# Optimization experiments

Hardware: AMD Instinct MI355X
Metric: run time of the kernel (lower is better)

## Reference

```python
import jax, jax.numpy as jnp
import numpy as np

SEQ_LEN = 4096
N_FEATURES = 1
EMB = 768
HID = 2 * EMB


def _lstm(x, Wih, Whh, bih, bhh):
    """PyTorch-semantics single-layer LSTM over x: [S, in] -> (hs [S, H], h_N [H]).
    Gate order: i, f, g, o. Zero initial state."""
    H = Whh.shape[1]
    # Precompute the input contribution for all timesteps (one big GEMM).
    xW = x @ Wih.T + (bih + bhh)  # [S, 4H]

    def step(carry, g_in):
        h, c = carry
        gates = g_in + Whh @ h  # [4H]
        i, f, g, o = jnp.split(gates, 4)
        c = jax.nn.sigmoid(f) * c + jax.nn.sigmoid(i) * jnp.tanh(g)
        h = jax.nn.sigmoid(o) * jnp.tanh(c)
        return (h, c), h

    init = (jnp.zeros((H,), x.dtype), jnp.zeros((H,), x.dtype))
    (hN, _), hs = jax.lax.scan(step, init, xW)
    return hs, hN


def setup_inputs() -> dict:
    key = jax.random.key(0)
    ks = iter(jax.random.split(key, 32))

    def u(shape, H):
        b = 1.0 / np.sqrt(H)  # PyTorch LSTM/Linear init: U(-1/sqrt(H), 1/sqrt(H))
        return jax.random.uniform(next(ks), shape, jnp.float32, -b, b)

    def lstm_params(in_dim, H):
        return (u((4 * H, in_dim), H), u((4 * H, H), H), u((4 * H,), H), u((4 * H,), H))

    e1_Wih, e1_Whh, e1_bih, e1_bhh = lstm_params(N_FEATURES, HID)
    e2_Wih, e2_Whh, e2_bih, e2_bhh = lstm_params(HID, EMB)
    d1_Wih, d1_Whh, d1_bih, d1_bhh = lstm_params(EMB, EMB)
    d2_Wih, d2_Whh, d2_bih, d2_bhh = lstm_params(EMB, HID)
    out_W = u((N_FEATURES, HID), HID)
    out_b = u((N_FEATURES,), HID)

    x = jax.random.normal(next(ks), (SEQ_LEN, N_FEATURES), jnp.float32)
    return dict(x=x,
                e1_Wih=e1_Wih, e1_Whh=e1_Whh, e1_bih=e1_bih, e1_bhh=e1_bhh,
                e2_Wih=e2_Wih, e2_Whh=e2_Whh, e2_bih=e2_bih, e2_bhh=e2_bhh,
                d1_Wih=d1_Wih, d1_Whh=d1_Whh, d1_bih=d1_bih, d1_bhh=d1_bhh,
                d2_Wih=d2_Wih, d2_Whh=d2_Whh, d2_bih=d2_bih, d2_bhh=d2_bhh,
                out_W=out_W, out_b=out_b)


def reference(x,
              e1_Wih, e1_Whh, e1_bih, e1_bhh,
              e2_Wih, e2_Whh, e2_bih, e2_bhh,
              d1_Wih, d1_Whh, d1_bih, d1_bhh,
              d2_Wih, d2_Whh, d2_bih, d2_bhh,
              out_W, out_b):
    x = x.reshape(SEQ_LEN, N_FEATURES)
    h1, _ = _lstm(x, e1_Wih, e1_Whh, e1_bih, e1_bhh)          # [S, HID]
    _, z = _lstm(h1, e2_Wih, e2_Whh, e2_bih, e2_bhh)          # [EMB] bottleneck
    zrep = jnp.broadcast_to(z, (SEQ_LEN, EMB))                # repeat across time
    d1, _ = _lstm(zrep, d1_Wih, d1_Whh, d1_bih, d1_bhh)       # [S, EMB]
    d2, _ = _lstm(d1, d2_Wih, d2_Whh, d2_bih, d2_bhh)         # [S, HID]
    return d2 @ out_W.T + out_b                               # [S, N_FEATURES]
```

## Files before the change

kernel.cpp:

```cpp
#include <hip/hip_runtime.h>
#include <math.h>
#include <stdint.h>

#define SEQ   4096
#define NWG   256
#define NTHR  256
#define FINTAG 0x40000000u

#define WS_BIG  0
#define WS_SML  12288
#define WS_FIN  18432
#define WS_OUTP 18944
#define WS_ZERO WS_OUTP

typedef float f32x4 __attribute__((ext_vector_type(4)));
typedef float f32x2 __attribute__((ext_vector_type(2)));

__device__ __forceinline__ float sigf(float x){
  float e = __builtin_amdgcn_exp2f(-1.44269504089f * x);
  return __builtin_amdgcn_rcpf(1.0f + e);
}
__device__ __forceinline__ float tanhf_fast(float x){
  float e = __builtin_amdgcn_exp2f(2.88539008178f * x);
  return 1.0f - 2.0f * __builtin_amdgcn_rcpf(e + 1.0f);
}

__device__ __forceinline__ float wsum64(float v){
#pragma unroll
  for (int m = 32; m > 0; m >>= 1) v += __shfl_xor(v, m);
  return v;
}

__device__ __forceinline__ float g_load(const float* p){
  return __hip_atomic_load(p, __ATOMIC_RELAXED, __HIP_MEMORY_SCOPE_AGENT);
}
__device__ __forceinline__ void g_store(float* p, float v){
  __hip_atomic_store(p, v, __ATOMIC_RELAXED, __HIP_MEMORY_SCOPE_AGENT);
}
__device__ __forceinline__ void cell_store(float* cell, float h, unsigned tag){
  unsigned long long pk = ((unsigned long long)tag << 32) | (unsigned long long)__float_as_uint(h);
  __hip_atomic_store((unsigned long long*)cell, pk, __ATOMIC_RELAXED, __HIP_MEMORY_SCOPE_AGENT);
}

#define DOT4(acc, wv4, hv4) \
  acc += (wv4)[0]*(hv4)[0] + (wv4)[1]*(hv4)[1] + (wv4)[2]*(hv4)[2] + (wv4)[3]*(hv4)[3];

#define RETRY_BIG(bbp, tgv)                                                  \
  for(;;){                                                                   \
    asm volatile(                                                            \
      "global_load_dwordx4 %0, %3, off sc0 sc1\n\t"                          \
      "global_load_dwordx4 %1, %3, off offset:1024 sc0 sc1\n\t"              \
      "global_load_dwordx4 %2, %3, off offset:2048 sc0 sc1\n\t"              \
      "s_waitcnt vmcnt(0)"                                                   \
      : "=&v"(B0), "=&v"(B1), "=&v"(B2)                                      \
      : "v"(bbp) : "memory");                                                \
    unsigned tgu = (unsigned)(tgv);                                          \
    bool ok = (__float_as_uint(B0[1])==tgu) & (__float_as_uint(B0[3])==tgu)  \
            & (__float_as_uint(B1[1])==tgu) & (__float_as_uint(B1[3])==tgu)  \
            & (__float_as_uint(B2[1])==tgu) & (__float_as_uint(B2[3])==tgu); \
    if (__all(ok)) break;                                                    \
    __builtin_amdgcn_s_sleep(1);                                             \
  }

#define RETRY_SML(sbp, sb2p, tgv)                                            \
  for(;;){                                                                   \
    asm volatile(                                                            \
      "global_load_dwordx4 %0, %2, off sc0 sc1\n\t"                          \
      "global_load_dwordx2 %1, %3, off sc0 sc1\n\t"                          \
      "s_waitcnt vmcnt(0)"                                                   \
      : "=&v"(S0), "=&v"(S1v)                                                \
      : "v"(sbp), "v"(sb2p) : "memory");                                     \
    unsigned tgu = (unsigned)(tgv);                                          \
    bool ok = (__float_as_uint(S0[1])==tgu) & (__float_as_uint(S0[3])==tgu)  \
            & (__float_as_uint(S1v[1])==tgu);                                \
    if (__all(ok)) break;                                                    \
    __builtin_amdgcn_s_sleep(1);                                             \
  }

__global__ void init_ws(float* ws){
  int i = threadIdx.x + blockIdx.x*blockDim.x;
  for (; i < WS_ZERO; i += blockDim.x*gridDim.x)
    __hip_atomic_store(ws + i, 0.0f, __ATOMIC_RELAXED, __HIP_MEMORY_SCOPE_AGENT);
}

__global__ __launch_bounds__(NTHR, 1) void lstm_ae(
    const float* __restrict__ x,
    const float* __restrict__ e1Wih, const float* __restrict__ e1Whh,
    const float* __restrict__ e1bih, const float* __restrict__ e1bhh,
    const float* __restrict__ e2Wih, const float* __restrict__ e2Whh,
    const float* __restrict__ e2bih, const float* __restrict__ e2bhh,
    const float* __restrict__ d1Wih, const float* __restrict__ d1Whh,
    const float* __restrict__ d1bih, const float* __restrict__ d1bhh,
    const float* __restrict__ d2Wih, const float* __restrict__ d2Whh,
    const float* __restrict__ d2bih, const float* __restrict__ d2bhh,
    const float* __restrict__ outW, const float* __restrict__ outb,
    float* __restrict__ out, float* __restrict__ ws)
{
  const int w    = blockIdx.x;
  const int tid  = threadIdx.x;
  const int lane = tid & 63;
  const int v    = tid >> 6;

  float* outp = ws + WS_OUTP;

  __shared__ float lx[SEQ];
  __shared__ float lhB[2][1536];
  __shared__ float lhS[2][768];
  __shared__ float lgB[24], lgS[12];

  for (int i = tid; i < SEQ; i += NTHR) lx[i] = x[i];

  f32x4 wR[6][6];
  f32x4 wA[18];
  f32x4 wB[9];
  float wihB[6], biasB[6], biasS[3], zw[3], bz[3];

#pragma unroll
  for (int r = 0; r < 6; ++r){
    const int row = v*1536 + 6*w + r;
    const float* p = e1Whh + (size_t)row*1536 + 4*lane;
#pragma unroll
    for (int q = 0; q < 6; ++q) wR[r][q] = *(const f32x4*)(p + 256*q);
    wihB[r]  = e1Wih[row];
    biasB[r] = e1bih[row] + e1bhh[row];
  }
#pragma unroll
  for (int r = 0; r < 3; ++r){
    const int row = v*768 + 3*w + r;
    const float* pi = e2Wih + (size_t)row*1536 + 4*lane;
#pragma unroll
    for (int q = 0; q < 6; ++q) wA[r*6+q] = *(const f32x4*)(pi + 256*q);
    const float* ph = e2Whh + (size_t)row*768 + 4*lane;
#pragma unroll
    for (int q = 0; q < 3; ++q) wB[r*3+q] = *(const f32x4*)(ph + 256*q);
    biasS[r] = e2bih[row] + e2bhh[row];
  }

  float cB = 0.0f, cS = 0.0f;
  const float ob = outb[0];
  float ow = (v == 0 && lane < 6) ? outW[6*w + lane] : 0.0f;

  __syncthreads();

  for (int g = 0; g <= SEQ; ++g){
    const int slot = g & 3, buf = g & 1;
    {
      const float* bb = ws + WS_BIG + slot*3072 + (384*v + 2*lane)*2;
      f32x4 B0,B1,B2;
      RETRY_BIG(bb, g);
      *(f32x2*)&lhB[buf][384*v +       2*lane] = f32x2{B0[0], B0[2]};
      *(f32x2*)&lhB[buf][384*v + 128 + 2*lane] = f32x2{B1[0], B1[2]};
      *(f32x2*)&lhB[buf][384*v + 256 + 2*lane] = f32x2{B2[0], B2[2]};
    }
    __syncthreads();

    if (g < SEQ){
      f32x4 H[6];
#pragma unroll
      for (int q = 0; q < 6; ++q) H[q] = *(const f32x4*)&lhB[buf][256*q + 4*lane];
      float a0=0.f,a1=0.f,a2=0.f,a3=0.f,a4=0.f,a5=0.f;
#pragma unroll
      for (int q = 0; q < 6; ++q){
        DOT4(a0, wR[0][q], H[q]); DOT4(a1, wR[1][q], H[q]); DOT4(a2, wR[2][q], H[q]);
        DOT4(a3, wR[3][q], H[q]); DOT4(a4, wR[4][q], H[q]); DOT4(a5, wR[5][q], H[q]);
      }
      a0=wsum64(a0); a1=wsum64(a1); a2=wsum64(a2);
      a3=wsum64(a3); a4=wsum64(a4); a5=wsum64(a5);
      if (lane == 0){
        float xt = lx[g];
        lgB[v*6+0]=a0+wihB[0]*xt+biasB[0]; lgB[v*6+1]=a1+wihB[1]*xt+biasB[1];
        lgB[v*6+2]=a2+wihB[2]*xt+biasB[2]; lgB[v*6+3]=a3+wihB[3]*xt+biasB[3];
        lgB[v*6+4]=a4+wihB[4]*xt+biasB[4]; lgB[v*6+5]=a5+wihB[5]*xt+biasB[5];
      }
    }
    __syncthreads();

    if (v == 0 && g < SEQ && lane < 6){
      float gi=lgB[lane],gf=lgB[6+lane],gg=lgB[12+lane],go=lgB[18+lane];
      cB = sigf(gf)*cB + sigf(gi)*tanhf_fast(gg);
      cell_store(ws + WS_BIG + ((g+1)&3)*3072 + (6*w+lane)*2,
                 sigf(go)*tanhf_fast(cB), (unsigned)(g+1));
    }

    if (g >= 1){
      const float* smlb = ws + WS_SML + slot*1536;
      const float* sb  = smlb + (192*v + 2*lane)*2;
      const float* sb2 = smlb + (192*v + 128 + lane)*2;
      f32x4 S0; f32x2 S1v;
      RETRY_SML(sb, sb2, g);
      *(f32x2*)&lhS[buf][192*v + 2*lane] = f32x2{S0[0], S0[2]};
      lhS[buf][192*v + 128 + lane] = S1v[0];
    }
    __syncthreads();

    if (g >= 1){
      f32x4 H[6], S[3];
#pragma unroll
      for (int q = 0; q < 6; ++q) H[q] = *(const f32x4*)&lhB[buf][256*q + 4*lane];
#pragma unroll
      for (int q = 0; q < 3; ++q) S[q] = *(const f32x4*)&lhS[buf][256*q + 4*lane];
      float b0=0.f,b1=0.f,b2=0.f;
#pragma unroll
      for (int q = 0; q < 6; ++q){
        DOT4(b0, wA[0*6+q], H[q]); DOT4(b1, wA[1*6+q], H[q]); DOT4(b2, wA[2*6+q], H[q]);
      }
#pragma unroll
      for (int q = 0; q < 3; ++q){
        DOT4(b0, wB[0*3+q], S[q]); DOT4(b1, wB[1*3+q], S[q]); DOT4(b2, wB[2*3+q], S[q]);
      }
      b0=wsum64(b0); b1=wsum64(b1); b2=wsum64(b2);
      if (lane == 0){
        lgS[v*3+0]=b0+biasS[0]; lgS[v*3+1]=b1+biasS[1]; lgS[v*3+2]=b2+biasS[2];
      }
    }
    __syncthreads();

    if (v == 0 && lane >= 8 && lane < 11){
      int u = lane - 8;
      float hv = 0.0f;
      if (g >= 1){
        float gi=lgS[u],gf=lgS[3+u],gg=lgS[6+u],go=lgS[9+u];
        cS = sigf(gf)*cS + sigf(gi)*tanhf_fast(gg);
        hv = sigf(go)*tanhf_fast(cS);
      }
      cell_store(ws + WS_SML + ((g+1)&3)*1536 + (3*w+u)*2, hv, (unsigned)(g+1));
    }
  }

  {
#pragma unroll
    for (int r = 0; r < 3; ++r){
      const int row = v*768 + 3*w + r;
      const float* p = d1Wih + (size_t)row*768 + 4*lane;
#pragma unroll
      for (int q = 0; q < 3; ++q) wB[r*3+q] = *(const f32x4*)(p + 256*q);
      bz[r] = d1bih[row] + d1bhh[row];
    }
    const int tg = SEQ+1, slot = tg & 3, buf = tg & 1;
    const float* smlb = ws + WS_SML + slot*1536;
    const float* sb  = smlb + (192*v + 2*lane)*2;
    const float* sb2 = smlb + (192*v + 128 + lane)*2;
    f32x4 S0; f32x2 S1v;
    RETRY_SML(sb, sb2, tg);
    *(f32x2*)&lhS[buf][192*v + 2*lane] = f32x2{S0[0], S0[2]};
    lhS[buf][192*v + 128 + lane] = S1v[0];
    __syncthreads();
    f32x4 S[3];
#pragma unroll
    for (int q = 0; q < 3; ++q) S[q] = *(const f32x4*)&lhS[buf][256*q + 4*lane];
    float z0=0.f,z1=0.f,z2=0.f;
#pragma unroll
    for (int q = 0; q < 3; ++q){
      DOT4(z0, wB[0*3+q], S[q]); DOT4(z1, wB[1*3+q], S[q]); DOT4(z2, wB[2*3+q], S[q]);
    }
    zw[0]=wsum64(z0)+bz[0]; zw[1]=wsum64(z1)+bz[1]; zw[2]=wsum64(z2)+bz[2];
  }

#pragma unroll
  for (int r = 0; r < 6; ++r){
    const int row = v*1536 + 6*w + r;
    const float* p = d2Whh + (size_t)row*1536 + 4*lane;
#pragma unroll
    for (int q = 0; q < 6; ++q) wR[r][q] = *(const f32x4*)(p + 256*q);
    const float* pi = d2Wih + (size_t)row*768 + 4*lane;
#pragma unroll
    for (int q = 0; q < 3; ++q) wA[r*3+q] = *(const f32x4*)(pi + 256*q);
    biasB[r] = d2bih[row] + d2bhh[row];
  }
#pragma unroll
  for (int r = 0; r < 3; ++r){
    const int row = v*768 + 3*w + r;
    const float* p = d1Whh + (size_t)row*768 + 4*lane;
#pragma unroll
    for (int q = 0; q < 3; ++q) wB[r*3+q] = *(const f32x4*)(p + 256*q);
  }
  cB = 0.0f; cS = 0.0f;

  for (int t = 0; t <= SEQ; ++t){
    const int pc = SEQ+1+t, slot = pc & 3, buf = pc & 1;
    if (t >= 1){
      const float* smlb = ws + WS_SML + slot*1536;
      const float* sb  = smlb + (192*v + 2*lane)*2;
      const float* sb2 = smlb + (192*v + 128 + lane)*2;
      f32x4 S0; f32x2 S1v;
      RETRY_SML(sb, sb2, pc);
      *(f32x2*)&lhS[buf][192*v + 2*lane] = f32x2{S0[0], S0[2]};
      lhS[buf][192*v + 128 + lane] = S1v[0];
    }
    __syncthreads();

    if (t < SEQ){
      f32x4 S[3];
      if (t >= 1){
#pragma unroll
        for (int q = 0; q < 3; ++q) S[q] = *(const f32x4*)&lhS[buf][256*q + 4*lane];
      } else {
#pragma unroll
        for (int q = 0; q < 3; ++q) S[q] = (f32x4)0.0f;
      }
      float b0=0.f,b1=0.f,b2=0.f;
#pragma unroll
      for (int q = 0; q < 3; ++q){
        DOT4(b0, wB[0*3+q], S[q]); DOT4(b1, wB[1*3+q], S[q]); DOT4(b2, wB[2*3+q], S[q]);
      }
      b0=wsum64(b0); b1=wsum64(b1); b2=wsum64(b2);
      if (lane == 0){
        lgS[v*3+0]=b0+zw[0]; lgS[v*3+1]=b1+zw[1]; lgS[v*3+2]=b2+zw[2];
      }
    }
    __syncthreads();

    if (v == 0){
      if (t < SEQ && lane >= 8 && lane < 11){
        int u = lane - 8;
        float gi=lgS[u],gf=lgS[3+u],gg=lgS[6+u],go=lgS[9+u];
        cS = sigf(gf)*cS + sigf(gi)*tanhf_fast(gg);
        cell_store(ws + WS_SML + ((pc+1)&3)*1536 + (3*w+u)*2,
                   sigf(go)*tanhf_fast(cS), (unsigned)(pc+1));
      }
      if (t == 0 && lane < 6)
        cell_store(ws + WS_BIG + ((pc+1)&3)*3072 + (6*w+lane)*2, 0.0f, (unsigned)(pc+1));
    }

    if (t >= 1){
      const float* bb = ws + WS_BIG + slot*3072 + (384*v + 2*lane)*2;
      f32x4 B0,B1,B2;
      RETRY_BIG(bb, pc);
      *(f32x2*)&lhB[buf][384*v +       2*lane] = f32x2{B0[0], B0[2]};
      *(f32x2*)&lhB[buf][384*v + 128 + 2*lane] = f32x2{B1[0], B1[2]};
      *(f32x2*)&lhB[buf][384*v + 256 + 2*lane] = f32x2{B2[0], B2[2]};
    }
    __syncthreads();

    if (t >= 1){
      f32x4 H[6], S[3];
#pragma unroll
      for (int q = 0; q < 6; ++q) H[q] = *(const f32x4*)&lhB[buf][256*q + 4*lane];
#pragma unroll
      for (int q = 0; q < 3; ++q) S[q] = *(const f32x4*)&lhS[buf][256*q + 4*lane];
      float a0=0.f,a1=0.f,a2=0.f,a3=0.f,a4=0.f,a5=0.f;
#pragma unroll
      for (int q = 0; q < 6; ++q){
        DOT4(a0, wR[0][q], H[q]); DOT4(a1, wR[1][q], H[q]); DOT4(a2, wR[2][q], H[q]);
        DOT4(a3, wR[3][q], H[q]); DOT4(a4, wR[4][q], H[q]); DOT4(a5, wR[5][q], H[q]);
      }
#pragma unroll
      for (int q = 0; q < 3; ++q){
        DOT4(a0, wA[0*3+q], S[q]); DOT4(a1, wA[1*3+q], S[q]); DOT4(a2, wA[2*3+q], S[q]);
        DOT4(a3, wA[3*3+q], S[q]); DOT4(a4, wA[4*3+q], S[q]); DOT4(a5, wA[5*3+q], S[q]);
      }
      a0=wsum64(a0); a1=wsum64(a1); a2=wsum64(a2);
      a3=wsum64(a3); a4=wsum64(a4); a5=wsum64(a5);
      if (lane == 0){
        lgB[v*6+0]=a0+biasB[0]; lgB[v*6+1]=a1+biasB[1]; lgB[v*6+2]=a2+biasB[2];
        lgB[v*6+3]=a3+biasB[3]; lgB[v*6+4]=a4+biasB[4]; lgB[v*6+5]=a5+biasB[5];
      }
    }
    __syncthreads();

    if (v == 0 && t >= 1){
      float vv = 0.0f;
      if (lane < 6){
        float gi=lgB[lane],gf=lgB[6+lane],gg=lgB[12+lane],go=lgB[18+lane];
        cB = sigf(gf)*cB + sigf(gi)*tanhf_fast(gg);
        float hv = sigf(go)*tanhf_fast(cB);
        cell_store(ws + WS_BIG + ((pc+1)&3)*3072 + (6*w+lane)*2, hv, (unsigned)(pc+1));
        vv = hv * ow;
      }
      if (lane < 8){
        vv += __shfl_xor(vv,1); vv += __shfl_xor(vv,2); vv += __shfl_xor(vv,4);
        if (lane == 0) g_store(&outp[(size_t)(t-1)*NWG + w], vv);
      }
    }
  }

  if (v == 0){
    asm volatile("s_waitcnt vmcnt(0)" ::: "memory");
    if (lane == 0) cell_store(ws + WS_FIN + w*2, 0.0f, FINTAG);
    const float* fb = ws + WS_FIN + (4*lane)*2;
    f32x4 F0, F1;
    for(;;){
      asm volatile(
        "global_load_dwordx4 %0, %2, off sc0 sc1\n\t"
        "global_load_dwordx4 %1, %2, off offset:16 sc0 sc1\n\t"
        "s_waitcnt vmcnt(0)"
        : "=&v"(F0), "=&v"(F1) : "v"(fb) : "memory");
      bool ok = (__float_as_uint(F0[1])==FINTAG)&(__float_as_uint(F0[3])==FINTAG)
              & (__float_as_uint(F1[1])==FINTAG)&(__float_as_uint(F1[3])==FINTAG);
      if (__all(ok)) break;
      __builtin_amdgcn_s_sleep(1);
    }
  }
  __syncthreads();
  {
    const int tau = w*16 + (tid >> 4);
    const int s4  = tid & 15;
    float s = 0.f;
#pragma unroll
    for (int j = 0; j < 16; ++j) s += g_load(&outp[(size_t)tau*NWG + s4 + 16*j]);
    s += __shfl_xor(s,8); s += __shfl_xor(s,4); s += __shfl_xor(s,2); s += __shfl_xor(s,1);
    if (s4 == 0) out[tau] = s + ob;
  }
}

extern "C" void kernel_launch(void* const* d_in, const int* in_sizes, int n_in,
                              void* d_out, int out_size, void* d_ws, size_t ws_size,
                              hipStream_t stream){
  (void)in_sizes; (void)n_in; (void)out_size; (void)ws_size;
  const float* x     = (const float*)d_in[0];
  const float* e1Wih = (const float*)d_in[1];
  const float* e1Whh = (const float*)d_in[2];
  const float* e1bih = (const float*)d_in[3];
  const float* e1bhh = (const float*)d_in[4];
  const float* e2Wih = (const float*)d_in[5];
  const float* e2Whh = (const float*)d_in[6];
  const float* e2bih = (const float*)d_in[7];
  const float* e2bhh = (const float*)d_in[8];
  const float* d1Wih = (const float*)d_in[9];
  const float* d1Whh = (const float*)d_in[10];
  const float* d1bih = (const float*)d_in[11];
  const float* d1bhh = (const float*)d_in[12];
  const float* d2Wih = (const float*)d_in[13];
  const float* d2Whh = (const float*)d_in[14];
  const float* d2bih = (const float*)d_in[15];
  const float* d2bhh = (const float*)d_in[16];
  const float* outW  = (const float*)d_in[17];
  const float* outb  = (const float*)d_in[18];
  float* out = (float*)d_out;
  float* ws  = (float*)d_ws;

  hipLaunchKernelGGL(init_ws, dim3(32), dim3(256), 0, stream, ws);

  hipLaunchKernelGGL(lstm_ae, dim3(NWG), dim3(NTHR), 0, stream,
                     x,
                     e1Wih, e1Whh, e1bih, e1bhh,
                     e2Wih, e2Whh, e2bih, e2bhh,
                     d1Wih, d1Whh, d1bih, d1bhh,
                     d2Wih, d2Whh, d2bih, d2bhh,
                     outW,  outb,  out,   ws);
}
```

Baseline: 24.96 ms.

## Map each wave to one hidden unit's four gates, removing gate-exchange barriers

The block grows from four to six waves, and each wave now owns all four gate rows (i,f,g,o) of one hidden unit. Each wave can then finish its cell update in registers after its own wave reductions, with no LDS gate scratch and no extra __syncthreads per timestep. The small layers use only three of the waves, and the output projection is reduced through a small shared array. The cost is more waves per workgroup on this persistent kernel, two of them idle during small-layer steps, plus redundant cell math across lanes.

```diff
diff --git a/kernel.cpp b/kernel.cpp
--- a/kernel.cpp
+++ b/kernel.cpp
@@ -4,7 +4,7 @@
 
 #define SEQ   4096
 #define NWG   256
-#define NTHR  256
+#define NTHR  384
 #define FINTAG 0x40000000u
 
 #define WS_BIG  0
@@ -45,34 +45,30 @@
 #define DOT4(acc, wv4, hv4) \
   acc += (wv4)[0]*(hv4)[0] + (wv4)[1]*(hv4)[1] + (wv4)[2]*(hv4)[2] + (wv4)[3]*(hv4)[3];
 
-#define RETRY_BIG(bbp, tgv)                                                  \
+#define RETRY_BIG2(bbp, tgv)                                                 \
   for(;;){                                                                   \
     asm volatile(                                                            \
-      "global_load_dwordx4 %0, %3, off sc0 sc1\n\t"                          \
-      "global_load_dwordx4 %1, %3, off offset:1024 sc0 sc1\n\t"              \
-      "global_load_dwordx4 %2, %3, off offset:2048 sc0 sc1\n\t"              \
+      "global_load_dwordx4 %0, %2, off sc0 sc1\n\t"                          \
+      "global_load_dwordx4 %1, %2, off offset:1024 sc0 sc1\n\t"              \
       "s_waitcnt vmcnt(0)"                                                   \
-      : "=&v"(B0), "=&v"(B1), "=&v"(B2)                                      \
+      : "=&v"(B0), "=&v"(B1)                                                 \
       : "v"(bbp) : "memory");                                                \
     unsigned tgu = (unsigned)(tgv);                                          \
     bool ok = (__float_as_uint(B0[1])==tgu) & (__float_as_uint(B0[3])==tgu)  \
-            & (__float_as_uint(B1[1])==tgu) & (__float_as_uint(B1[3])==tgu)  \
-            & (__float_as_uint(B2[1])==tgu) & (__float_as_uint(B2[3])==tgu); \
+            & (__float_as_uint(B1[1])==tgu) & (__float_as_uint(B1[3])==tgu); \
     if (__all(ok)) break;                                                    \
     __builtin_amdgcn_s_sleep(1);                                             \
   }
 
-#define RETRY_SML(sbp, sb2p, tgv)                                            \
+#define RETRY_SML1(sbp, tgv)                                                 \
   for(;;){                                                                   \
     asm volatile(                                                            \
-      "global_load_dwordx4 %0, %2, off sc0 sc1\n\t"                          \
-      "global_load_dwordx2 %1, %3, off sc0 sc1\n\t"                          \
+      "global_load_dwordx4 %0, %1, off sc0 sc1\n\t"                          \
       "s_waitcnt vmcnt(0)"                                                   \
-      : "=&v"(S0), "=&v"(S1v)                                                \
-      : "v"(sbp), "v"(sb2p) : "memory");                                     \
+      : "=&v"(S0)                                                            \
+      : "v"(sbp) : "memory");                                                \
     unsigned tgu = (unsigned)(tgv);                                          \
-    bool ok = (__float_as_uint(S0[1])==tgu) & (__float_as_uint(S0[3])==tgu)  \
-            & (__float_as_uint(S1v[1])==tgu);                                \
+    bool ok = (__float_as_uint(S0[1])==tgu) & (__float_as_uint(S0[3])==tgu); \
     if (__all(ok)) break;                                                    \
     __builtin_amdgcn_s_sleep(1);                                             \
   }
@@ -106,51 +102,51 @@
   __shared__ float lx[SEQ];
   __shared__ float lhB[2][1536];
   __shared__ float lhS[2][768];
-  __shared__ float lgB[24], lgS[12];
+  __shared__ float lgS[12];
+  __shared__ float lops[6];
 
   for (int i = tid; i < SEQ; i += NTHR) lx[i] = x[i];
 
-  f32x4 wR[6][6];
-  f32x4 wA[18];
-  f32x4 wB[9];
-  float wihB[6], biasB[6], biasS[3], zw[3], bz[3];
-
-#pragma unroll
-  for (int r = 0; r < 6; ++r){
-    const int row = v*1536 + 6*w + r;
+  f32x4 wR[4][6];
+  float wihB[4], biasB[4];
+#pragma unroll
+  for (int k = 0; k < 4; ++k){
+    const int row = k*1536 + 6*w + v;
     const float* p = e1Whh + (size_t)row*1536 + 4*lane;
 #pragma unroll
-    for (int q = 0; q < 6; ++q) wR[r][q] = *(const f32x4*)(p + 256*q);
-    wihB[r]  = e1Wih[row];
-    biasB[r] = e1bih[row] + e1bhh[row];
-  }
-#pragma unroll
-  for (int r = 0; r < 3; ++r){
-    const int row = v*768 + 3*w + r;
+    for (int q = 0; q < 6; ++q) wR[k][q] = *(const f32x4*)(p + 256*q);
+    wihB[k]  = e1Wih[row];
+    biasB[k] = e1bih[row] + e1bhh[row];
+  }
+  f32x4 wA[2][6], wB2[2][3];
+  float biasS[2];
+#pragma unroll
+  for (int j = 0; j < 2; ++j){
+    const int idx = 2*v + j;
+    const int row = (idx/3)*768 + 3*w + (idx%3);
     const float* pi = e2Wih + (size_t)row*1536 + 4*lane;
 #pragma unroll
-    for (int q = 0; q < 6; ++q) wA[r*6+q] = *(const f32x4*)(pi + 256*q);
+    for (int q = 0; q < 6; ++q) wA[j][q] = *(const f32x4*)(pi + 256*q);
     const float* ph = e2Whh + (size_t)row*768 + 4*lane;
 #pragma unroll
-    for (int q = 0; q < 3; ++q) wB[r*3+q] = *(const f32x4*)(ph + 256*q);
-    biasS[r] = e2bih[row] + e2bhh[row];
-  }
-
-  float cB = 0.0f, cS = 0.0f;
+    for (int q = 0; q < 3; ++q) wB2[j][q] = *(const f32x4*)(ph + 256*q);
+    biasS[j] = e2bih[row] + e2bhh[row];
+  }
+
+  float cB = 0.0f;
+  float cS = 0.0f;
   const float ob = outb[0];
-  float ow = (v == 0 && lane < 6) ? outW[6*w + lane] : 0.0f;
 
   __syncthreads();
 
   for (int g = 0; g <= SEQ; ++g){
     const int slot = g & 3, buf = g & 1;
     {
-      const float* bb = ws + WS_BIG + slot*3072 + (384*v + 2*lane)*2;
-      f32x4 B0,B1,B2;
-      RETRY_BIG(bb, g);
-      *(f32x2*)&lhB[buf][384*v +       2*lane] = f32x2{B0[0], B0[2]};
-      *(f32x2*)&lhB[buf][384*v + 128 + 2*lane] = f32x2{B1[0], B1[2]};
-      *(f32x2*)&lhB[buf][384*v + 256 + 2*lane] = f32x2{B2[0], B2[2]};
+      const float* bb = ws + WS_BIG + slot*3072 + (256*v + 2*lane)*2;
+      f32x4 B0, B1;
+      RETRY_BIG2(bb, g);
+      *(f32x2*)&lhB[buf][256*v +       2*lane] = f32x2{B0[0], B0[2]};
+      *(f32x2*)&lhB[buf][256*v + 128 + 2*lane] = f32x2{B1[0], B1[2]};
     }
     __syncthreads();
 
@@ -158,38 +154,29 @@
       f32x4 H[6];
 #pragma unroll
       for (int q = 0; q < 6; ++q) H[q] = *(const f32x4*)&lhB[buf][256*q + 4*lane];
-      float a0=0.f,a1=0.f,a2=0.f,a3=0.f,a4=0.f,a5=0.f;
+      float a0=0.f,a1=0.f,a2=0.f,a3=0.f;
 #pragma unroll
       for (int q = 0; q < 6; ++q){
-        DOT4(a0, wR[0][q], H[q]); DOT4(a1, wR[1][q], H[q]); DOT4(a2, wR[2][q], H[q]);
-        DOT4(a3, wR[3][q], H[q]); DOT4(a4, wR[4][q], H[q]); DOT4(a5, wR[5][q], H[q]);
-      }
-      a0=wsum64(a0); a1=wsum64(a1); a2=wsum64(a2);
-      a3=wsum64(a3); a4=wsum64(a4); a5=wsum64(a5);
-      if (lane == 0){
-        float xt = lx[g];
-        lgB[v*6+0]=a0+wihB[0]*xt+biasB[0]; lgB[v*6+1]=a1+wihB[1]*xt+biasB[1];
-        lgB[v*6+2]=a2+wihB[2]*xt+biasB[2]; lgB[v*6+3]=a3+wihB[3]*xt+biasB[3];
-        lgB[v*6+4]=a4+wihB[4]*xt+biasB[4]; lgB[v*6+5]=a5+wihB[5]*xt+biasB[5];
-      }
-    }
-    __syncthreads();
-
-    if (v == 0 && g < SEQ && lane < 6){
-      float gi=lgB[lane],gf=lgB[6+lane],gg=lgB[12+lane],go=lgB[18+lane];
+        DOT4(a0, wR[0][q], H[q]); DOT4(a1, wR[1][q], H[q]);
+        DOT4(a2, wR[2][q], H[q]); DOT4(a3, wR[3][q], H[q]);
+      }
+      a0=wsum64(a0); a1=wsum64(a1); a2=wsum64(a2); a3=wsum64(a3);
+      float xt = lx[g];
+      float gi = a0 + wihB[0]*xt + biasB[0];
+      float gf = a1 + wihB[1]*xt + biasB[1];
+      float gg = a2 + wihB[2]*xt + biasB[2];
+      float go = a3 + wihB[3]*xt + biasB[3];
       cB = sigf(gf)*cB + sigf(gi)*tanhf_fast(gg);
-      cell_store(ws + WS_BIG + ((g+1)&3)*3072 + (6*w+lane)*2,
-                 sigf(go)*tanhf_fast(cB), (unsigned)(g+1));
+      float hv = sigf(go)*tanhf_fast(cB);
+      if (lane == 0)
+        cell_store(ws + WS_BIG + ((g+1)&3)*3072 + (6*w+v)*2, hv, (unsigned)(g+1));
     }
 
     if (g >= 1){
-      const float* smlb = ws + WS_SML + slot*1536;
-      const float* sb  = smlb + (192*v + 2*lane)*2;
-      const float* sb2 = smlb + (192*v + 128 + lane)*2;
-      f32x4 S0; f32x2 S1v;
-      RETRY_SML(sb, sb2, g);
-      *(f32x2*)&lhS[buf][192*v + 2*lane] = f32x2{S0[0], S0[2]};
-      lhS[buf][192*v + 128 + lane] = S1v[0];
+      const float* sb = ws + WS_SML + slot*1536 + (128*v + 2*lane)*2;
+      f32x4 S0;
+      RETRY_SML1(sb, g);
+      *(f32x2*)&lhS[buf][128*v + 2*lane] = f32x2{S0[0], S0[2]};
     }
     __syncthreads();
 
@@ -199,97 +186,97 @@
       for (int q = 0; q < 6; ++q) H[q] = *(const f32x4*)&lhB[buf][256*q + 4*lane];
 #pragma unroll
       for (int q = 0; q < 3; ++q) S[q] = *(const f32x4*)&lhS[buf][256*q + 4*lane];
-      float b0=0.f,b1=0.f,b2=0.f;
-#pragma unroll
-      for (int q = 0; q < 6; ++q){
-        DOT4(b0, wA[0*6+q], H[q]); DOT4(b1, wA[1*6+q], H[q]); DOT4(b2, wA[2*6+q], H[q]);
-      }
-#pragma unroll
-      for (int q = 0; q < 3; ++q){
-        DOT4(b0, wB[0*3+q], S[q]); DOT4(b1, wB[1*3+q], S[q]); DOT4(b2, wB[2*3+q], S[q]);
-      }
-      b0=wsum64(b0); b1=wsum64(b1); b2=wsum64(b2);
-      if (lane == 0){
-        lgS[v*3+0]=b0+biasS[0]; lgS[v*3+1]=b1+biasS[1]; lgS[v*3+2]=b2+biasS[2];
-      }
-    }
-    __syncthreads();
-
-    if (v == 0 && lane >= 8 && lane < 11){
-      int u = lane - 8;
+      float b0=0.f, b1=0.f;
+#pragma unroll
+      for (int q = 0; q < 6; ++q){ DOT4(b0, wA[0][q], H[q]); DOT4(b1, wA[1][q], H[q]); }
+#pragma unroll
+      for (int q = 0; q < 3; ++q){ DOT4(b0, wB2[0][q], S[q]); DOT4(b1, wB2[1][q], S[q]); }
+      b0 = wsum64(b0); b1 = wsum64(b1);
+      if (lane == 0){ lgS[2*v] = b0 + biasS[0]; lgS[2*v+1] = b1 + biasS[1]; }
+    }
+    __syncthreads();
+
+    if (v == 0 && lane < 3){
       float hv = 0.0f;
       if (g >= 1){
-        float gi=lgS[u],gf=lgS[3+u],gg=lgS[6+u],go=lgS[9+u];
+        float gi=lgS[lane], gf=lgS[3+lane], gg=lgS[6+lane], go=lgS[9+lane];
         cS = sigf(gf)*cS + sigf(gi)*tanhf_fast(gg);
         hv = sigf(go)*tanhf_fast(cS);
       }
-      cell_store(ws + WS_SML + ((g+1)&3)*1536 + (3*w+u)*2, hv, (unsigned)(g+1));
-    }
-  }
-
+      cell_store(ws + WS_SML + ((g+1)&3)*1536 + (3*w+lane)*2, hv, (unsigned)(g+1));
+    }
+  }
+
+  f32x4 wZ[4][3]; float bz[4];
+  if (v < 3){
+#pragma unroll
+    for (int k = 0; k < 4; ++k){
+      const int row = k*768 + 3*w + v;
+      const float* p = d1Wih + (size_t)row*768 + 4*lane;
+#pragma unroll
+      for (int q = 0; q < 3; ++q) wZ[k][q] = *(const f32x4*)(p + 256*q);
+      bz[k] = d1bih[row] + d1bhh[row];
+    }
+  }
+  float zw0=0.f, zw1=0.f, zw2=0.f, zw3=0.f;
   {
-#pragma unroll
-    for (int r = 0; r < 3; ++r){
-      const int row = v*768 + 3*w + r;
-      const float* p = d1Wih + (size_t)row*768 + 4*lane;
-#pragma unroll
-      for (int q = 0; q < 3; ++q) wB[r*3+q] = *(const f32x4*)(p + 256*q);
-      bz[r] = d1bih[row] + d1bhh[row];
-    }
-    const int tg = SEQ+1, slot = tg & 3, buf = tg & 1;
-    const float* smlb = ws + WS_SML + slot*1536;
-    const float* sb  = smlb + (192*v + 2*lane)*2;
-    const float* sb2 = smlb + (192*v + 128 + lane)*2;
-    f32x4 S0; f32x2 S1v;
-    RETRY_SML(sb, sb2, tg);
-    *(f32x2*)&lhS[buf][192*v + 2*lane] = f32x2{S0[0], S0[2]};
-    lhS[buf][192*v + 128 + lane] = S1v[0];
-    __syncthreads();
-    f32x4 S[3];
-#pragma unroll
-    for (int q = 0; q < 3; ++q) S[q] = *(const f32x4*)&lhS[buf][256*q + 4*lane];
-    float z0=0.f,z1=0.f,z2=0.f;
-#pragma unroll
-    for (int q = 0; q < 3; ++q){
-      DOT4(z0, wB[0*3+q], S[q]); DOT4(z1, wB[1*3+q], S[q]); DOT4(z2, wB[2*3+q], S[q]);
-    }
-    zw[0]=wsum64(z0)+bz[0]; zw[1]=wsum64(z1)+bz[1]; zw[2]=wsum64(z2)+bz[2];
-  }
-
-#pragma unroll
-  for (int r = 0; r < 6; ++r){
-    const int row = v*1536 + 6*w + r;
+    const int tg = SEQ+1, slot = tg & 3, buf2 = tg & 1;
+    const float* sb = ws + WS_SML + slot*1536 + (128*v + 2*lane)*2;
+    f32x4 S0;
+    RETRY_SML1(sb, tg);
+    *(f32x2*)&lhS[buf2][128*v + 2*lane] = f32x2{S0[0], S0[2]};
+    __syncthreads();
+    if (v < 3){
+      f32x4 S[3];
+#pragma unroll
+      for (int q = 0; q < 3; ++q) S[q] = *(const f32x4*)&lhS[buf2][256*q + 4*lane];
+      float z0=0.f,z1=0.f,z2=0.f,z3=0.f;
+#pragma unroll
+      for (int q = 0; q < 3; ++q){
+        DOT4(z0, wZ[0][q], S[q]); DOT4(z1, wZ[1][q], S[q]);
+        DOT4(z2, wZ[2][q], S[q]); DOT4(z3, wZ[3][q], S[q]);
+      }
+      zw0 = wsum64(z0) + bz[0]; zw1 = wsum64(z1) + bz[1];
+      zw2 = wsum64(z2) + bz[2]; zw3 = wsum64(z3) + bz[3];
+    }
+  }
+
+  f32x4 wA2[4][3];
+#pragma unroll
+  for (int k = 0; k < 4; ++k){
+    const int row = k*1536 + 6*w + v;
     const float* p = d2Whh + (size_t)row*1536 + 4*lane;
 #pragma unroll
-    for (int q = 0; q < 6; ++q) wR[r][q] = *(const f32x4*)(p + 256*q);
+    for (int q = 0; q < 6; ++q) wR[k][q] = *(const f32x4*)(p + 256*q);
     const float* pi = d2Wih + (size_t)row*768 + 4*lane;
 #pragma unroll
-    for (int q = 0; q < 3; ++q) wA[r*3+q] = *(const f32x4*)(pi + 256*q);
-    biasB[r] = d2bih[row] + d2bhh[row];
-  }
-#pragma unroll
-  for (int r = 0; r < 3; ++r){
-    const int row = v*768 + 3*w + r;
-    const float* p = d1Whh + (size_t)row*768 + 4*lane;
-#pragma unroll
-    for (int q = 0; q < 3; ++q) wB[r*3+q] = *(const f32x4*)(p + 256*q);
-  }
+    for (int q = 0; q < 3; ++q) wA2[k][q] = *(const f32x4*)(pi + 256*q);
+    biasB[k] = d2bih[row] + d2bhh[row];
+  }
+  f32x4 wD1[4][3];
+  if (v < 3){
+#pragma unroll
+    for (int k = 0; k < 4; ++k){
+      const int row = k*768 + 3*w + v;
+      const float* p = d1Whh + (size_t)row*768 + 4*lane;
+#pragma unroll
+      for (int q = 0; q < 3; ++q) wD1[k][q] = *(const f32x4*)(p + 256*q);
+    }
+  }
+  const float ow = outW[6*w + v];
   cB = 0.0f; cS = 0.0f;
 
   for (int t = 0; t <= SEQ; ++t){
     const int pc = SEQ+1+t, slot = pc & 3, buf = pc & 1;
     if (t >= 1){
-      const float* smlb = ws + WS_SML + slot*1536;
-      const float* sb  = smlb + (192*v + 2*lane)*2;
-      const float* sb2 = smlb + (192*v + 128 + lane)*2;
-      f32x4 S0; f32x2 S1v;
-      RETRY_SML(sb, sb2, pc);
-      *(f32x2*)&lhS[buf][192*v + 2*lane] = f32x2{S0[0], S0[2]};
-      lhS[buf][192*v + 128 + lane] = S1v[0];
-    }
-    __syncthreads();
-
-    if (t < SEQ){
+      const float* sb = ws + WS_SML + slot*1536 + (128*v + 2*lane)*2;
+      f32x4 S0;
+      RETRY_SML1(sb, pc);
+      *(f32x2*)&lhS[buf][128*v + 2*lane] = f32x2{S0[0], S0[2]};
+    }
+    __syncthreads();
+
+    if (t < SEQ && v < 3){
       f32x4 S[3];
       if (t >= 1){
 #pragma unroll
@@ -298,37 +285,28 @@
 #pragma unroll
         for (int q = 0; q < 3; ++q) S[q] = (f32x4)0.0f;
       }
-      float b0=0.f,b1=0.f,b2=0.f;
+      float d0=0.f,d1v=0.f,d2v=0.f,d3=0.f;
 #pragma unroll
       for (int q = 0; q < 3; ++q){
-        DOT4(b0, wB[0*3+q], S[q]); DOT4(b1, wB[1*3+q], S[q]); DOT4(b2, wB[2*3+q], S[q]);
-      }
-      b0=wsum64(b0); b1=wsum64(b1); b2=wsum64(b2);
-      if (lane == 0){
-        lgS[v*3+0]=b0+zw[0]; lgS[v*3+1]=b1+zw[1]; lgS[v*3+2]=b2+zw[2];
-      }
-    }
-    __syncthreads();
-
-    if (v == 0){
-      if (t < SEQ && lane >= 8 && lane < 11){
-        int u = lane - 8;
-        float gi=lgS[u],gf=lgS[3+u],gg=lgS[6+u],go=lgS[9+u];
-        cS = sigf(gf)*cS + sigf(gi)*tanhf_fast(gg);
-        cell_store(ws + WS_SML + ((pc+1)&3)*1536 + (3*w+u)*2,
-                   sigf(go)*tanhf_fast(cS), (unsigned)(pc+1));
-      }
-      if (t == 0 && lane < 6)
-        cell_store(ws + WS_BIG + ((pc+1)&3)*3072 + (6*w+lane)*2, 0.0f, (unsigned)(pc+1));
-    }
+        DOT4(d0, wD1[0][q], S[q]); DOT4(d1v, wD1[1][q], S[q]);
+        DOT4(d2v, wD1[2][q], S[q]); DOT4(d3, wD1[3][q], S[q]);
+      }
+      d0=wsum64(d0); d1v=wsum64(d1v); d2v=wsum64(d2v); d3=wsum64(d3);
+      float gi = d0 + zw0, gf = d1v + zw1, gg = d2v + zw2, go = d3 + zw3;
+      cS = sigf(gf)*cS + sigf(gi)*tanhf_fast(gg);
+      float hv = sigf(go)*tanhf_fast(cS);
+      if (lane == 0)
+        cell_store(ws + WS_SML + ((pc+1)&3)*1536 + (3*w+v)*2, hv, (unsigned)(pc+1));
+    }
+    if (t == 0 && v == 0 && lane < 6)
+      cell_store(ws + WS_BIG + ((pc+1)&3)*3072 + (6*w+lane)*2, 0.0f, (unsigned)(pc+1));
 
     if (t >= 1){
-      const float* bb = ws + WS_BIG + slot*3072 + (384*v + 2*lane)*2;
-      f32x4 B0,B1,B2;
-      RETRY_BIG(bb, pc);
-      *(f32x2*)&lhB[buf][384*v +       2*lane] = f32x2{B0[0], B0[2]};
-      *(f32x2*)&lhB[buf][384*v + 128 + 2*lane] = f32x2{B1[0], B1[2]};
-      *(f32x2*)&lhB[buf][384*v + 256 + 2*lane] = f32x2{B2[0], B2[2]};
+      const float* bb = ws + WS_BIG + slot*3072 + (256*v + 2*lane)*2;
+      f32x4 B0, B1;
+      RETRY_BIG2(bb, pc);
+      *(f32x2*)&lhB[buf][256*v +       2*lane] = f32x2{B0[0], B0[2]};
+      *(f32x2*)&lhB[buf][256*v + 128 + 2*lane] = f32x2{B1[0], B1[2]};
     }
     __syncthreads();
 
@@ -338,40 +316,31 @@
       for (int q = 0; q < 6; ++q) H[q] = *(const f32x4*)&lhB[buf][256*q + 4*lane];
 #pragma unroll
       for (int q = 0; q < 3; ++q) S[q] = *(const f32x4*)&lhS[buf][256*q + 4*lane];
-      float a0=0.f,a1=0.f,a2=0.f,a3=0.f,a4=0.f,a5=0.f;
+      float a0=0.f,a1=0.f,a2=0.f,a3=0.f;
 #pragma unroll
       for (int q = 0; q < 6; ++q){
-        DOT4(a0, wR[0][q], H[q]); DOT4(a1, wR[1][q], H[q]); DOT4(a2, wR[2][q], H[q]);
-        DOT4(a3, wR[3][q], H[q]); DOT4(a4, wR[4][q], H[q]); DOT4(a5, wR[5][q], H[q]);
+        DOT4(a0, wR[0][q], H[q]); DOT4(a1, wR[1][q], H[q]);
+        DOT4(a2, wR[2][q], H[q]); DOT4(a3, wR[3][q], H[q]);
       }
 #pragma unroll
       for (int q = 0; q < 3; ++q){
-        DOT4(a0, wA[0*3+q], S[q]); DOT4(a1, wA[1*3+q], S[q]); DOT4(a2, wA[2*3+q], S[q]);
-        DOT4(a3, wA[3*3+q], S[q]); DOT4(a4, wA[4*3+q], S[q]); DOT4(a5, wA[5*3+q], S[q]);
-      }
-      a0=wsum64(a0); a1=wsum64(a1); a2=wsum64(a2);
-      a3=wsum64(a3); a4=wsum64(a4); a5=wsum64(a5);
+        DOT4(a0, wA2[0][q], S[q]); DOT4(a1, wA2[1][q], S[q]);
+        DOT4(a2, wA2[2][q], S[q]); DOT4(a3, wA2[3][q], S[q]);
+      }
+      a0=wsum64(a0); a1=wsum64(a1); a2=wsum64(a2); a3=wsum64(a3);
+      float gi = a0 + biasB[0], gf = a1 + biasB[1];
+      float gg = a2 + biasB[2], go = a3 + biasB[3];
+      cB = sigf(gf)*cB + sigf(gi)*tanhf_fast(gg);
+      float hv = sigf(go)*tanhf_fast(cB);
       if (lane == 0){
-        lgB[v*6+0]=a0+biasB[0]; lgB[v*6+1]=a1+biasB[1]; lgB[v*6+2]=a2+biasB[2];
-        lgB[v*6+3]=a3+biasB[3]; lgB[v*6+4]=a4+biasB[4]; lgB[v*6+5]=a5+biasB[5];
-      }
-    }
-    __syncthreads();
-
-    if (v == 0 && t >= 1){
-      float vv = 0.0f;
-      if (lane < 6){
-        float gi=lgB[lane],gf=lgB[6+lane],gg=lgB[12+lane],go=lgB[18+lane];
-        cB = sigf(gf)*cB + sigf(gi)*tanhf_fast(gg);
-        float hv = sigf(go)*tanhf_fast(cB);
-        cell_store(ws + WS_BIG + ((pc+1)&3)*3072 + (6*w+lane)*2, hv, (unsigned)(pc+1));
-        vv = hv * ow;
-      }
-      if (lane < 8){
-        vv += __shfl_xor(vv,1); vv += __shfl_xor(vv,2); vv += __shfl_xor(vv,4);
-        if (lane == 0) g_store(&outp[(size_t)(t-1)*NWG + w], vv);
-      }
-    }
+        cell_store(ws + WS_BIG + ((pc+1)&3)*3072 + (6*w+v)*2, hv, (unsigned)(pc+1));
+        lops[v] = hv * ow;
+      }
+    }
+    __syncthreads();
+    if (t >= 1 && tid == 0)
+      g_store(&outp[(size_t)(t-1)*NWG + w],
+              lops[0]+lops[1]+lops[2]+lops[3]+lops[4]+lops[5]);
   }
 
   if (v == 0){
@@ -392,7 +361,7 @@
     }
   }
   __syncthreads();
-  {
+  if (tid < 256){
     const int tau = w*16 + (tid >> 4);
     const int s4  = tid & 15;
     float s = 0.f;
```

Result: slower. 29.87 ms (+19.7%).
